# Optimization experiments

Measured on AMD Instinct MI355X. Metric: run time of the kernel, lower is better.

Reference implementation:

```python
import jax, jax.numpy as jnp
import numpy as np

N, C, H, W = 8, 80, 200, 200
PRE_NMS_THRESH = 0.05
PRE_NMS_TOP_N = 1000
NMS_THRESH = 0.6
FPN_POST_NMS_TOP_N = 100
MIN_SIZE = 0.0
TO_REMOVE = 1.0
CLASS_OFFSET = 100000.0  # > any coordinate; separates classes for class-aware NMS


def setup_inputs() -> dict:
    key = jax.random.key(0)
    k1, k2, k3, k4, k5 = jax.random.split(key, 5)
    # logits shifted so sigmoid probs sit near the 0.05 threshold (realistic sparsity)
    box_cls = jax.random.normal(k1, (N, C, H, W), jnp.float32) - 3.0
    box_regression = jax.random.uniform(k2, (N, 4, H, W), jnp.float32) * 64.0
    centerness = jax.random.normal(k3, (N, 1, H, W), jnp.float32)
    locations = jax.random.uniform(k4, (H * W, 2), jnp.float32) * 1600.0
    image_sizes = jax.random.randint(k5, (N, 2), 800, 1600, jnp.int32)  # (h, w)
    return {"locations": locations, "box_cls": box_cls,
            "box_regression": box_regression, "centerness": centerness,
            "image_sizes": image_sizes}


def _pairwise_iou(boxes):
    x1, y1, x2, y2 = boxes[:, 0], boxes[:, 1], boxes[:, 2], boxes[:, 3]
    area = (x2 - x1 + TO_REMOVE) * (y2 - y1 + TO_REMOVE)  # [K]
    iw = jnp.clip(jnp.minimum(x2[:, None], x2[None, :]) - jnp.maximum(x1[:, None], x1[None, :]) + TO_REMOVE, 0.0)
    ih = jnp.clip(jnp.minimum(y2[:, None], y2[None, :]) - jnp.maximum(y1[:, None], y1[None, :]) + TO_REMOVE, 0.0)
    inter = iw * ih
    return inter / (area[:, None] + area[None, :] - inter)


def reference(locations, box_cls, box_regression, centerness, image_sizes):
    n, c, h, w = box_cls.shape
    # [N,C,H,W] -> [N,HW,C] probs; [N,4,H,W] -> [N,HW,4]; centerness -> [N,HW]
    cls_prob = jax.nn.sigmoid(box_cls.transpose(0, 2, 3, 1).reshape(n, -1, c))
    reg = box_regression.transpose(0, 2, 3, 1).reshape(n, -1, 4)
    cent = jax.nn.sigmoid(centerness.transpose(0, 2, 3, 1).reshape(n, -1))

    def per_image(p, r, ct, hw):
        # candidate mask on raw class probs (before centerness weighting), as in source
        cand = p > PRE_NMS_THRESH                      # [HW, C]
        scores = p * ct[:, None]                       # [HW, C]
        flat = jnp.where(cand, scores, -jnp.inf).reshape(-1)
        top_s, top_i = jax.lax.top_k(flat, PRE_NMS_TOP_N)   # sorted desc
        loc_idx = top_i // c
        labels = top_i % c + 1
        valid = top_s > 0.0
        l2 = locations[loc_idx]                        # [K, 2]
        rr = r[loc_idx]                                # [K, 4]
        boxes = jnp.concatenate([l2 - rr[:, :2], l2 + rr[:, 2:]], axis=-1)
        ih = hw[0].astype(jnp.float32)
        iw = hw[1].astype(jnp.float32)
        boxes = jnp.stack([jnp.clip(boxes[:, 0], 0.0, iw - 1.0),
                           jnp.clip(boxes[:, 1], 0.0, ih - 1.0),
                           jnp.clip(boxes[:, 2], 0.0, iw - 1.0),
                           jnp.clip(boxes[:, 3], 0.0, ih - 1.0)], axis=-1)
        bw = boxes[:, 2] - boxes[:, 0] + TO_REMOVE
        bh = boxes[:, 3] - boxes[:, 1] + TO_REMOVE
        valid = valid & (bw >= MIN_SIZE) & (bh >= MIN_SIZE)
        # class-aware NMS via per-class coordinate offset
        ob = boxes + labels.astype(jnp.float32)[:, None] * CLASS_OFFSET
        iou = _pairwise_iou(ob)                        # [K, K]
        K = PRE_NMS_TOP_N
        idxs = jnp.arange(K)
        def body(supp, i):
            keep_i = valid[i] & jnp.logical_not(supp[i])
            supp = supp | (keep_i & (iou[i] > NMS_THRESH) & (idxs != i))
            return supp, keep_i
        _, keep = jax.lax.scan(body, jnp.zeros(K, dtype=bool), idxs)
        fscores = jnp.where(keep & valid, top_s, -jnp.inf)
        fs, fi = jax.lax.top_k(fscores, FPN_POST_NMS_TOP_N)
        fv = fs > 0.0
        fb = boxes[fi] * fv[:, None].astype(boxes.dtype)
        fl = jnp.where(fv, labels[fi], 0).astype(jnp.float32)
        out_s = jnp.where(fv, jnp.sqrt(jnp.where(fv, fs, 1.0)), 0.0)  # sqrt of cls*centerness
        # [K_post, 6] = x1,y1,x2,y2,score,label
        return jnp.concatenate([fb, out_s[:, None], fl[:, None]], axis=-1)

    return jax.vmap(per_image)(cls_prob, reg, cent, image_sizes)
```

## Files before the change

### kernel.cpp

```cpp
#include <hip/hip_runtime.h>
#include <math.h>

#define NIMG 8
#define NCLS 80
#define HW 40000
#define M (NCLS*HW)
#define UBINS 4096
#define CANDL 4096
#define SPILL_CAP 65536
#define BCAP 1024
#define TOPK 1000
#define OUTK 100
#define PRE_T 0.05f
#define NMS_T 0.6f
#define FLOOR_S 0.25f
#define FLOOR_BITS 0x3E800000u
#define FLOOR_SAFE 0.2494f

__device__ unsigned int       g_scnt[NIMG][32];
__device__ unsigned int       g_ovf[NIMG];
__device__ float              g_xthr[NIMG * HW];
__device__ float              g_sct[NIMG * HW];
__device__ unsigned long long g_key[NIMG][SPILL_CAP];

__device__ __forceinline__ float sigmoid_exact(float x){
    return 1.0f / (1.0f + expf(-x));
}

__device__ __forceinline__ unsigned long long shfl_xor_u64(unsigned long long v, int j){
    int lo = __shfl_xor((int)(unsigned int)(v & 0xffffffffull), j);
    int hi = __shfl_xor((int)(unsigned int)(v >> 32), j);
    return ((unsigned long long)(unsigned int)hi << 32) | (unsigned long long)(unsigned int)lo;
}

__global__ void k0_init(const float* __restrict__ cent){
    int t = blockIdx.x * blockDim.x + threadIdx.x;
    if (t < NIMG * 32) ((unsigned int*)g_scnt)[t] = 0u;
    if (t < NIMG) g_ovf[t] = 0u;
    if (t < NIMG * HW){
        float pct = sigmoid_exact(cent[t]);
        g_sct[t] = pct;
        float a = FLOOR_SAFE / pct;
        float xt;
        if (a >= 1.0f) xt = 3.0e38f;
        else {
            float am = fminf(a, 0.98f);
            xt = logf(am / (1.0f - am));
        }
        g_xthr[t] = xt;
    }
}

__global__ void __launch_bounds__(1024) k1_spill(const float* __restrict__ cls){
    const int n   = blockIdx.y;
    const int tid = threadIdx.x;
    const int e0  = blockIdx.x * 4096 + tid * 4;
    __shared__ unsigned long long skey[BCAP];
    __shared__ unsigned int lcnt, lbase;
    if (tid == 0) lcnt = 0u;
    __syncthreads();
    if (e0 < M){
        const int c  = e0 / HW;
        const int hw = e0 - c * HW;
        float4 x  = *(const float4*)(cls + (size_t)n * M + e0);
        float4 th = *(const float4*)(g_xthr + n * HW + hw);
        #define SPILL1(J, XV) \
        if (XV >= (J==0?th.x:J==1?th.y:J==2?th.z:th.w)){ \
            float p_ = sigmoid_exact(XV); \
            if (p_ > PRE_T){ \
                float s_ = p_ * g_sct[n * HW + hw + J]; \
                unsigned long long key_ = ((unsigned long long)__float_as_uint(s_) << 32) \
                    | (unsigned long long)(0xFFFFFFFFu - (unsigned int)((hw + J) * NCLS + c)); \
                unsigned int pp_ = atomicAdd(&lcnt, 1u); \
                if (pp_ < BCAP) skey[pp_] = key_; \
            } \
        }
        SPILL1(0, x.x)
        SPILL1(1, x.y)
        SPILL1(2, x.z)
        SPILL1(3, x.w)
        #undef SPILL1
    }
    __syncthreads();
    unsigned int raw = lcnt;
    unsigned int cnt = raw < BCAP ? raw : BCAP;
    if (tid == 0){
        lbase = cnt ? atomicAdd(&g_scnt[n][0], cnt) : 0u;
        if (raw > BCAP) g_ovf[n] = 1u;
    }
    __syncthreads();
    unsigned int base = lbase;
    for (unsigned int i = tid; i < cnt; i += 1024){
        unsigned int pos = base + i;
        if (pos < SPILL_CAP) g_key[n][pos] = skey[i];
    }
}

struct SelPhase {
    unsigned int hist[UBINS];
    unsigned int cs[256];
    unsigned long long keysL[CANDL];
};
struct NmsPhase {
    float ox1[TOPK], oy1[TOPK], ox2[TOPK], oy2[TOPK], oar[TOPK];
    float bxs[TOPK][4];
    float sc[TOPK];
    int   lab[TOPK];
    int   keeplist[OUTK];
    unsigned int  Wc[16][80];
    unsigned int  ctot[80];
    unsigned int  coff[81];
    unsigned int  wcnt[16];
    unsigned short ord[1024];
    unsigned char validf[TOPK];
    unsigned char supp[TOPK];
    unsigned char keepf[1024];
};
union KU { SelPhase sel; NmsPhase nms; };

#define REGSTEP(K_, J_) { \
    unsigned long long pa = shfl_xor_u64(va, (J_)); \
    unsigned long long pb = shfl_xor_u64(vb, (J_)); \
    bool fa = ((tid & (J_)) == 0); \
    bool da = ((tid & (K_)) == 0); \
    bool db = (((tid + 1024) & (K_)) == 0); \
    va = (fa == da) ? (va > pa ? va : pa) : (va < pa ? va : pa); \
    vb = (fa == db) ? (vb > pb ? vb : pb) : (vb < pb ? vb : pb); \
}

__global__ void __launch_bounds__(1024) k2_select_nms(const float* __restrict__ cls,
                                                      const float* __restrict__ loc,
                                                      const float* __restrict__ reg,
                                                      const int*   __restrict__ imsz,
                                                      float* __restrict__ out){
    const int n = blockIdx.x;
    const int tid = threadIdx.x;
    const int lane = tid & 63;
    const int wv   = tid >> 6;
    __shared__ KU u;
    __shared__ unsigned long long stop[TOPK];
    __shared__ unsigned int lcnt, c025, s_cut, s_flag, s_nmsfb, s_cnt, s_aok;

    if (tid == 0){ s_nmsfb = 0u; }

    unsigned int scnt_raw = g_scnt[n][0];
    unsigned int ovf_f    = g_ovf[n];
    unsigned int S = scnt_raw < SPILL_CAP ? scnt_raw : SPILL_CAP;

    bool modeA = (!ovf_f) && (scnt_raw >= TOPK) && (scnt_raw <= 2048);
    unsigned long long kk = 0ull;
    bool needBC = true;

    if (modeA){
        unsigned long long va = ((unsigned int)tid < S) ? g_key[n][tid] : 0ull;
        unsigned long long vb = ((unsigned int)(tid + 1024) < S) ? g_key[n][tid + 1024] : 0ull;

        REGSTEP(2,1)
        REGSTEP(4,2)  REGSTEP(4,1)
        REGSTEP(8,4)  REGSTEP(8,2)  REGSTEP(8,1)
        REGSTEP(16,8) REGSTEP(16,4) REGSTEP(16,2) REGSTEP(16,1)
        REGSTEP(32,16) REGSTEP(32,8) REGSTEP(32,4) REGSTEP(32,2) REGSTEP(32,1)
        REGSTEP(64,32) REGSTEP(64,16) REGSTEP(64,8) REGSTEP(64,4) REGSTEP(64,2) REGSTEP(64,1)

        for (int k = 128; k <= 2048; k <<= 1){
            if (k == 2048){
                unsigned long long mx = va > vb ? va : vb;
                unsigned long long mn = va > vb ? vb : va;
                va = mx; vb = mn;
            }
            u.sel.keysL[tid] = va; u.sel.keysL[tid + 1024] = vb;
            __syncthreads();
            for (int j = (k == 2048) ? 512 : (k >> 1); j >= 64; j >>= 1){
                int i  = ((tid & ~(j - 1)) << 1) | (tid & (j - 1));
                int l  = i | j;
                unsigned long long a = u.sel.keysL[i];
                unsigned long long b = u.sel.keysL[l];
                bool up = ((i & k) == 0);
                if (up ? (a < b) : (a > b)){ u.sel.keysL[i] = b; u.sel.keysL[l] = a; }
                __syncthreads();
            }
            va = u.sel.keysL[tid]; vb = u.sel.keysL[tid + 1024];
            REGSTEP(k,32) REGSTEP(k,16) REGSTEP(k,8) REGSTEP(k,4) REGSTEP(k,2) REGSTEP(k,1)
        }
        if (tid == TOPK - 1) s_aok = (((unsigned int)(va >> 32)) >= FLOOR_BITS) ? 1u : 0u;
        kk = (tid < TOPK) ? va : 0ull;
        __syncthreads();
        needBC = (s_aok == 0u);
    }

    if (needBC){
        for (int i = tid; i < UBINS; i += 1024) u.sel.hist[i] = 0u;
        if (tid == 0){ lcnt = 0u; c025 = 0u; }
        if (tid < TOPK) stop[tid] = 0ull;
        __syncthreads();

        for (unsigned int i = tid; i < S; i += 1024){
            unsigned long long k = g_key[n][i];
            unsigned int bits = (unsigned int)(k >> 32);
            float s = __uint_as_float(bits);
            int bin = (int)(s * 4096.0f);
            atomicAdd(&u.sel.hist[bin], 1u);
            unsigned long long mb = __ballot(bits >= FLOOR_BITS);
            if (lane == 0 && mb) atomicAdd(&c025, (unsigned int)__popcll(mb));
        }
        __syncthreads();
        if (tid < 256){
            unsigned int s = 0;
            int base = tid * 16;
            #pragma unroll
            for (int i = 0; i < 16; ++i) s += u.sel.hist[base + i];
            u.sel.cs[tid] = s;
        }
        __syncthreads();
        if (tid == 0){
            unsigned int acc = 0; int cut = 0;
            int c = 255;
            for (; c >= 0; --c){ if (acc + u.sel.cs[c] >= TOPK) break; acc += u.sel.cs[c]; }
            unsigned int Cest = 0;
            if (c >= 0){
                int b = c*16 + 15;
                for (;; --b){
                    if (acc + u.sel.hist[b] >= TOPK || b == c*16){ cut = b; break; }
                    acc += u.sel.hist[b];
                }
                Cest = acc + u.sel.hist[cut];
            }
            unsigned int fl = (scnt_raw > SPILL_CAP) || ovf_f || (c < 0) ||
                              (c025 < TOPK) || (Cest > CANDL) ? 1u : 0u;
            s_cut = (unsigned int)cut; s_flag = fl;
        }
        __syncthreads();

        if (s_flag){
            for (int i = tid; i < UBINS; i += 1024) u.sel.hist[i] = 0u;
            __syncthreads();
            const float* cls_n = cls + (size_t)n * M;
            const float* sct_n = g_sct + n * HW;
            for (int e = tid; e < M; e += 1024){
                float p = sigmoid_exact(cls_n[e]);
                if (p > PRE_T){
                    int c = e / HW; int hw = e - c * HW;
                    float s = p * sct_n[hw];
                    atomicAdd(&u.sel.hist[(int)(s * 4096.0f)], 1u);
                }
            }
            __syncthreads();
            if (tid < 256){
                unsigned int s = 0;
                int base = tid * 16;
                #pragma unroll
                for (int i = 0; i < 16; ++i) s += u.sel.hist[base + i];
                u.sel.cs[tid] = s;
            }
            __syncthreads();
            if (tid == 0){
                unsigned int acc = 0; int cut = 0; int c = 255;
                for (; c >= 0; --c){ if (acc + u.sel.cs[c] >= TOPK) break; acc += u.sel.cs[c]; }
                if (c >= 0){
                    int b = c*16 + 15;
                    for (;; --b){ acc += u.sel.hist[b]; if (acc >= TOPK || b == c*16) break; }
                    cut = b;
                }
                while (acc > CANDL && cut < UBINS){ acc -= u.sel.hist[cut]; cut++; }
                s_cut = (unsigned int)cut;
            }
            __syncthreads();
            unsigned int cutb = s_cut;
            for (int e = tid; e < M; e += 1024){
                float p = sigmoid_exact(cls_n[e]);
                if (p > PRE_T){
                    int c = e / HW; int hw = e - c * HW;
                    float s = p * sct_n[hw];
                    if ((int)(s * 4096.0f) >= (int)cutb){
                        unsigned int pos = atomicAdd(&lcnt, 1u);
                        if (pos < CANDL){
                            unsigned int idx = (unsigned int)(hw * NCLS + c);
                            u.sel.keysL[pos] = ((unsigned long long)__float_as_uint(s) << 32)
                                             | (unsigned long long)(0xFFFFFFFFu - idx);
                        }
                    }
                }
            }
        } else {
            unsigned int cutb = s_cut;
            for (unsigned int i = tid; i < S; i += 1024){
                unsigned long long k = g_key[n][i];
                float s = __uint_as_float((unsigned int)(k >> 32));
                bool pass = ((unsigned int)(int)(s * 4096.0f)) >= cutb;
                unsigned long long mb = __ballot(pass);
                unsigned int wcnt_ = (unsigned int)__popcll(mb);
                unsigned int base = 0;
                if (lane == 0 && wcnt_) base = atomicAdd(&lcnt, wcnt_);
                base = (unsigned int)__builtin_amdgcn_readfirstlane((int)base);
                if (pass){
                    unsigned int p = base + (unsigned int)__popcll(mb & ((1ull << lane) - 1ull));
                    if (p < CANDL) u.sel.keysL[p] = k;
                }
            }
        }
        __syncthreads();

        int C = (int)(lcnt < CANDL ? lcnt : CANDL);
        if (C <= 2048){
            int Nsort = (C <= 1024) ? 1024 : 2048;
            for (int i = C + tid; i < Nsort; i += 1024) u.sel.keysL[i] = 0ull;
            __syncthreads();
            for (int k = 2; k <= Nsort; k <<= 1){
                for (int j = k >> 1; j > 0; j >>= 1){
                    if (tid < (Nsort >> 1)){
                        int i  = ((tid & ~(j - 1)) << 1) | (tid & (j - 1));
                        int p2 = i | j;
                        unsigned long long a = u.sel.keysL[i];
                        unsigned long long b = u.sel.keysL[p2];
                        bool up = ((i & k) == 0);
                        if (up ? (a < b) : (a > b)){ u.sel.keysL[i] = b; u.sel.keysL[p2] = a; }
                    }
                    __syncthreads();
                }
            }
            if (tid < TOPK) stop[tid] = u.sel.keysL[tid];
        } else {
            for (int i = tid; i < C; i += 1024){
                unsigned long long k = u.sel.keysL[i];
                int rank = 0;
                for (int j = 0; j < C; ++j) rank += (u.sel.keysL[j] > k) ? 1 : 0;
                if (rank < TOPK) stop[rank] = k;
            }
        }
        __syncthreads();
        kk = (tid < TOPK) ? stop[tid] : 0ull;
        __syncthreads();
    }

    float rx1 = 0.f, ry1 = 0.f, rx2 = -1.f, ry2 = -1.f, rar = 1.f;
    float ihh = (float)imsz[2*n + 0];
    float iww = (float)imsz[2*n + 1];

    u.nms.keepf[tid] = 0;
    { unsigned int* wz = &u.nms.Wc[0][0];
      for (int i = tid; i < 16*80; i += 1024) wz[i] = 0u; }

    if (tid < TOPK){
        unsigned int bits = (unsigned int)(kk >> 32);
        float s = __uint_as_float(bits);
        u.nms.supp[tid] = 0;
        if (s > 0.0f){
            unsigned int idx = 0xFFFFFFFFu - (unsigned int)(kk & 0xFFFFFFFFull);
            int hw = (int)(idx / NCLS);
            int c  = (int)(idx % NCLS);
            int l  = c + 1;
            float x  = loc[2*hw], y = loc[2*hw + 1];
            float r0 = reg[((size_t)n*4 + 0)*HW + hw];
            float r1 = reg[((size_t)n*4 + 1)*HW + hw];
            float r2 = reg[((size_t)n*4 + 2)*HW + hw];
            float r3 = reg[((size_t)n*4 + 3)*HW + hw];
            float x1 = fminf(fmaxf(x - r0, 0.0f), iww - 1.0f);
            float y1 = fminf(fmaxf(y - r1, 0.0f), ihh - 1.0f);
            float x2 = fminf(fmaxf(x + r2, 0.0f), iww - 1.0f);
            float y2 = fminf(fmaxf(y + r3, 0.0f), ihh - 1.0f);
            u.nms.bxs[tid][0] = x1; u.nms.bxs[tid][1] = y1;
            u.nms.bxs[tid][2] = x2; u.nms.bxs[tid][3] = y2;
            float off = (float)l * 100000.0f;
            float a1 = x1 + off, b1 = y1 + off, a2 = x2 + off, b2 = y2 + off;
            float ar = (a2 - a1 + 1.0f) * (b2 - b1 + 1.0f);
            u.nms.ox1[tid] = a1; u.nms.oy1[tid] = b1;
            u.nms.ox2[tid] = a2; u.nms.oy2[tid] = b2; u.nms.oar[tid] = ar;
            rx1 = a1; ry1 = b1; rx2 = a2; ry2 = b2; rar = ar;
            u.nms.sc[tid] = s; u.nms.lab[tid] = l; u.nms.validf[tid] = 1;
        } else {
            u.nms.validf[tid] = 0; u.nms.sc[tid] = 0.0f; u.nms.lab[tid] = 0;
            u.nms.bxs[tid][0] = u.nms.bxs[tid][1] = 0.0f;
            u.nms.bxs[tid][2] = u.nms.bxs[tid][3] = 0.0f;
            u.nms.ox1[tid] = 0.f; u.nms.oy1[tid] = 0.f;
            u.nms.ox2[tid] = -1.f; u.nms.oy2[tid] = -1.f; u.nms.oar[tid] = 1.f;
        }
    }
    __syncthreads();

    int mk = -1;
    if (tid < TOPK && u.nms.validf[tid]) mk = u.nms.lab[tid] - 1;
    if (mk >= 0) atomicAdd(&u.nms.Wc[wv][mk], 1u);
    __syncthreads();
    if (tid < NCLS){
        unsigned int acc = 0;
        for (int w = 0; w < 16; ++w){
            unsigned int v = u.nms.Wc[w][tid];
            u.nms.Wc[w][tid] = acc;
            acc += v;
        }
        u.nms.ctot[tid] = acc;
        if (acc > 64) atomicOr(&s_nmsfb, 1u);
    }
    __syncthreads();
    if (tid <= NCLS){
        unsigned int acc = 0;
        for (int kq = 0; kq < tid; ++kq) acc += u.nms.ctot[kq];
        u.nms.coff[tid] = acc;
    }
    __syncthreads();

    if (!s_nmsfb){
        int below = 0;
        for (int l = 0; l < 64; ++l){
            int ok = __shfl(mk, l);
            below += (l < lane && ok == mk) ? 1 : 0;
        }
        if (mk >= 0){
            unsigned int pos = u.nms.coff[mk] + u.nms.Wc[wv][mk] + (unsigned int)below;
            u.nms.ord[pos] = (unsigned short)tid;
        }
        __syncthreads();

        for (int k = wv; k < NCLS; k += 16){
            int base = (int)u.nms.coff[k];
            int ck   = (int)u.nms.coff[k + 1] - base;
            if (ck <= 0) continue;
            int rr = (lane < ck) ? (int)u.nms.ord[base + lane] : -1;
            float bx1 = 0.f, by1 = 0.f, bx2 = -1.f, by2 = -1.f, bar = 1.f;
            if (rr >= 0){
                bx1 = u.nms.ox1[rr]; by1 = u.nms.oy1[rr];
                bx2 = u.nms.ox2[rr]; by2 = u.nms.oy2[rr]; bar = u.nms.oar[rr];
            }
            int sup = 0;
            for (int p = 0; p < ck; ++p){
                int keep_p = !__shfl(sup, p);
                if (keep_p){
                    float px1 = __shfl(bx1, p), py1 = __shfl(by1, p);
                    float px2 = __shfl(bx2, p), py2 = __shfl(by2, p);
                    float par = __shfl(bar, p);
                    if (lane > p && rr >= 0){
                        float ix1 = fmaxf(px1, bx1);
                        float iy1 = fmaxf(py1, by1);
                        float ix2 = fminf(px2, bx2);
                        float iy2 = fminf(py2, by2);
                        float iw_ = fmaxf(ix2 - ix1 + 1.0f, 0.0f);
                        float ih_ = fmaxf(iy2 - iy1 + 1.0f, 0.0f);
                        float inter = iw_ * ih_;
                        float iou = inter / (par + bar - inter);
                        if (iou > NMS_T) sup = 1;
                    }
                }
            }
            if (rr >= 0) u.nms.keepf[rr] = sup ? 0 : 1;
        }
        __syncthreads();

        int kf = (int)u.nms.keepf[tid];
        unsigned long long mb = __ballot(kf != 0);
        if (lane == 0) u.nms.wcnt[wv] = (unsigned int)__popcll(mb);
        __syncthreads();
        if (wv == 0){
            unsigned int v = (lane < 16) ? u.nms.wcnt[lane] : 0u;
            unsigned int orig = v;
            for (int d = 1; d < 16; d <<= 1){
                unsigned int t = __shfl_up(v, d);
                if (lane >= d) v += t;
            }
            if (lane < 16) u.nms.wcnt[lane] = v - orig;
            if (lane == 15) s_cnt = (v < OUTK ? v : OUTK);
        }
        __syncthreads();
        if (kf){
            unsigned int slot = u.nms.wcnt[wv] + (unsigned int)__popcll(mb & ((1ull << lane) - 1ull));
            if (slot < OUTK) u.nms.keeplist[slot] = tid;
        }
    } else {
        int cnt = 0;
        for (int i = 0; i < TOPK; ++i){
            bool keep_i = u.nms.validf[i] && !u.nms.supp[i];
            if (keep_i){
                if (tid == 0) u.nms.keeplist[cnt] = i;
                if (tid < TOPK && tid != i){
                    float ix1 = fmaxf(u.nms.ox1[i], rx1);
                    float iy1 = fmaxf(u.nms.oy1[i], ry1);
                    float ix2 = fminf(u.nms.ox2[i], rx2);
                    float iy2 = fminf(u.nms.oy2[i], ry2);
                    float iw_ = fmaxf(ix2 - ix1 + 1.0f, 0.0f);
                    float ih_ = fmaxf(iy2 - iy1 + 1.0f, 0.0f);
                    float inter = iw_ * ih_;
                    float iou = inter / (u.nms.oar[i] + rar - inter);
                    if (iou > NMS_T) u.nms.supp[tid] = 1;
                }
                cnt++;
                __syncthreads();
                if (cnt == OUTK) break;
            }
        }
        if (tid == 0) s_cnt = (unsigned int)(cnt < OUTK ? cnt : OUTK);
    }
    __syncthreads();

    int cnt = (int)s_cnt;
    if (tid < OUTK){
        float r0=0.f,r1=0.f,r2=0.f,r3=0.f,r4=0.f,r5=0.f;
        if (tid < cnt){
            int i = u.nms.keeplist[tid];
            r0 = u.nms.bxs[i][0]; r1 = u.nms.bxs[i][1];
            r2 = u.nms.bxs[i][2]; r3 = u.nms.bxs[i][3];
            r4 = sqrtf(u.nms.sc[i]); r5 = (float)u.nms.lab[i];
        }
        float* o = out + ((size_t)n*OUTK + tid)*6;
        o[0]=r0; o[1]=r1; o[2]=r2; o[3]=r3; o[4]=r4; o[5]=r5;
    }
}

extern "C" void kernel_launch(void* const* d_in, const int* in_sizes, int n_in,
                              void* d_out, int out_size, void* d_ws, size_t ws_size,
                              hipStream_t stream){
    const float* loc  = (const float*)d_in[0];
    const float* cls  = (const float*)d_in[1];
    const float* reg  = (const float*)d_in[2];
    const float* cent = (const float*)d_in[3];
    const int*   imsz = (const int*)d_in[4];
    float* out = (float*)d_out;

    hipLaunchKernelGGL(k0_init,       dim3(625),                 dim3(512),  0, stream, cent);
    hipLaunchKernelGGL(k1_spill,      dim3((M+4095)/4096, NIMG), dim3(1024), 0, stream, cls);
    hipLaunchKernelGGL(k2_select_nms, dim3(NIMG),                dim3(1024), 0, stream,
                       cls, loc, reg, imsz, out);
}
```

Measured before the change: 254.6 us.

## Unify selection path with parallel histogram scans and sort-verify fallback

Restructures top-K selection so the spilled-key histogram and cutoff search always run first. Serial single-thread scans for the bin cutoff and class offsets become wave-level shuffle prefix sums. Candidates above the cutoff are then sorted with the register/LDS hybrid bitonic sort, followed by a sortedness check that falls back to the full shared-memory bitonic sort if needed. This drops the speculative mode-A path and its floor re-check, trading an extra histogram pass for fewer serial loops and fewer divergent code paths.

```diff
diff --git a/kernel.cpp b/kernel.cpp
--- a/kernel.cpp
+++ b/kernel.cpp
@@ -13,7 +13,6 @@
 #define OUTK 100
 #define PRE_T 0.05f
 #define NMS_T 0.6f
-#define FLOOR_S 0.25f
 #define FLOOR_BITS 0x3E800000u
 #define FLOOR_SAFE 0.2494f
 
@@ -99,6 +98,7 @@
 struct SelPhase {
     unsigned int hist[UBINS];
     unsigned int cs[256];
+    unsigned int wtot[4];
     unsigned long long keysL[CANDL];
 };
 struct NmsPhase {
@@ -139,29 +139,158 @@
     const int wv   = tid >> 6;
     __shared__ KU u;
     __shared__ unsigned long long stop[TOPK];
-    __shared__ unsigned int lcnt, c025, s_cut, s_flag, s_nmsfb, s_cnt, s_aok;
-
-    if (tid == 0){ s_nmsfb = 0u; }
+    __shared__ unsigned int lcnt, s_cut, s_flag, s_nmsfb, s_cnt, s_c, s_csn, s_Cest, s_srtbad;
+
+    for (int i = tid; i < UBINS; i += 1024) u.sel.hist[i] = 0u;
+    if (tid == 0){ s_nmsfb = 0u; s_srtbad = 0u; s_c = 0xFFFFFFFFu; s_csn = 0u;
+                   s_Cest = 0u; s_cut = 0u; lcnt = 0u; }
+    if (tid < TOPK) stop[tid] = 0ull;
+    __syncthreads();
 
     unsigned int scnt_raw = g_scnt[n][0];
     unsigned int ovf_f    = g_ovf[n];
     unsigned int S = scnt_raw < SPILL_CAP ? scnt_raw : SPILL_CAP;
 
-    bool modeA = (!ovf_f) && (scnt_raw >= TOPK) && (scnt_raw <= 2048);
+    for (unsigned int i = tid; i < S; i += 1024){
+        unsigned long long k = g_key[n][i];
+        float s = __uint_as_float((unsigned int)(k >> 32));
+        atomicAdd(&u.sel.hist[(int)(s * 4096.0f)], 1u);
+    }
+    __syncthreads();
+    if (tid < 256){
+        unsigned int s = 0;
+        int base = tid * 16;
+        #pragma unroll
+        for (int i = 0; i < 16; ++i) s += u.sel.hist[base + i];
+        u.sel.cs[tid] = s;
+    }
+    __syncthreads();
+    if (tid < 256){
+        unsigned int v = u.sel.cs[tid];
+        #pragma unroll
+        for (int d = 1; d < 64; d <<= 1){
+            unsigned int t = __shfl_down(v, d);
+            if (lane + d < 64) v += t;
+        }
+        if (lane == 0) u.sel.wtot[wv] = v;
+        u.sel.cs[tid] = v;
+    }
+    __syncthreads();
+    if (tid < 256){
+        unsigned int tail = 0;
+        for (int w = wv + 1; w < 4; ++w) tail += u.sel.wtot[w];
+        u.sel.cs[tid] += tail;
+    }
+    __syncthreads();
+    if (tid < 256){
+        unsigned int a = u.sel.cs[tid];
+        unsigned int b = (tid == 255) ? 0u : u.sel.cs[tid + 1];
+        if (a >= TOPK && b < TOPK){ s_c = (unsigned int)tid; s_csn = b; }
+    }
+    __syncthreads();
+    if (wv == 0 && s_c != 0xFFFFFFFFu){
+        unsigned int cst = s_c;
+        unsigned int h = (lane < 16) ? u.sel.hist[cst * 16 + lane] : 0u;
+        #pragma unroll
+        for (int d = 1; d < 16; d <<= 1){
+            unsigned int t = __shfl_down(h, d);
+            if (lane + d < 16) h += t;
+        }
+        unsigned int gs  = h + s_csn;
+        unsigned int gsn = __shfl_down(gs, 1);
+        if (lane == 15) gsn = s_csn;
+        if (lane < 16 && gs >= TOPK && gsn < TOPK){ s_cut = cst * 16 + lane; s_Cest = gs; }
+    }
+    __syncthreads();
+    if (tid == 0){
+        unsigned int c025 = u.sel.cs[64];
+        s_flag = (scnt_raw > SPILL_CAP) || ovf_f || (s_c == 0xFFFFFFFFu) ||
+                 (c025 < TOPK) || (s_Cest > CANDL) ? 1u : 0u;
+    }
+    __syncthreads();
+
+    if (s_flag){
+        for (int i = tid; i < UBINS; i += 1024) u.sel.hist[i] = 0u;
+        __syncthreads();
+        const float* cls_n = cls + (size_t)n * M;
+        const float* sct_n = g_sct + n * HW;
+        for (int e = tid; e < M; e += 1024){
+            float p = sigmoid_exact(cls_n[e]);
+            if (p > PRE_T){
+                int c = e / HW; int hw = e - c * HW;
+                float s = p * sct_n[hw];
+                atomicAdd(&u.sel.hist[(int)(s * 4096.0f)], 1u);
+            }
+        }
+        __syncthreads();
+        if (tid < 256){
+            unsigned int s = 0;
+            int base = tid * 16;
+            #pragma unroll
+            for (int i = 0; i < 16; ++i) s += u.sel.hist[base + i];
+            u.sel.cs[tid] = s;
+        }
+        __syncthreads();
+        if (tid == 0){
+            unsigned int acc = 0; int cut = 0; int c = 255;
+            for (; c >= 0; --c){ if (acc + u.sel.cs[c] >= TOPK) break; acc += u.sel.cs[c]; }
+            if (c >= 0){
+                int b = c*16 + 15;
+                for (;; --b){ acc += u.sel.hist[b]; if (acc >= TOPK || b == c*16) break; }
+                cut = b;
+            }
+            while (acc > CANDL && cut < UBINS){ acc -= u.sel.hist[cut]; cut++; }
+            s_cut = (unsigned int)cut;
+        }
+        __syncthreads();
+        unsigned int cutb = s_cut;
+        for (int e = tid; e < M; e += 1024){
+            float p = sigmoid_exact(cls_n[e]);
+            if (p > PRE_T){
+                int c = e / HW; int hw = e - c * HW;
+                float s = p * sct_n[hw];
+                if ((int)(s * 4096.0f) >= (int)cutb){
+                    unsigned int pos = atomicAdd(&lcnt, 1u);
+                    if (pos < CANDL){
+                        unsigned int idx = (unsigned int)(hw * NCLS + c);
+                        u.sel.keysL[pos] = ((unsigned long long)__float_as_uint(s) << 32)
+                                         | (unsigned long long)(0xFFFFFFFFu - idx);
+                    }
+                }
+            }
+        }
+    } else {
+        unsigned int cutb = s_cut;
+        for (unsigned int i = tid; i < S; i += 1024){
+            unsigned long long k = g_key[n][i];
+            float s = __uint_as_float((unsigned int)(k >> 32));
+            bool pass = ((unsigned int)(int)(s * 4096.0f)) >= cutb;
+            unsigned long long mb = __ballot(pass);
+            unsigned int wcnt_ = (unsigned int)__popcll(mb);
+            unsigned int base = 0;
+            if (lane == 0 && wcnt_) base = atomicAdd(&lcnt, wcnt_);
+            base = (unsigned int)__builtin_amdgcn_readfirstlane((int)base);
+            if (pass){
+                unsigned int p = base + (unsigned int)__popcll(mb & ((1ull << lane) - 1ull));
+                if (p < CANDL) u.sel.keysL[p] = k;
+            }
+        }
+    }
+    __syncthreads();
+
+    int C = (int)(lcnt < CANDL ? lcnt : CANDL);
     unsigned long long kk = 0ull;
-    bool needBC = true;
-
-    if (modeA){
-        unsigned long long va = ((unsigned int)tid < S) ? g_key[n][tid] : 0ull;
-        unsigned long long vb = ((unsigned int)(tid + 1024) < S) ? g_key[n][tid + 1024] : 0ull;
-
+    if (C <= 2048){
+        for (int i = C + tid; i < 2048; i += 1024) u.sel.keysL[i] = 0ull;
+        __syncthreads();
+        unsigned long long va = u.sel.keysL[tid];
+        unsigned long long vb = u.sel.keysL[tid + 1024];
         REGSTEP(2,1)
         REGSTEP(4,2)  REGSTEP(4,1)
         REGSTEP(8,4)  REGSTEP(8,2)  REGSTEP(8,1)
         REGSTEP(16,8) REGSTEP(16,4) REGSTEP(16,2) REGSTEP(16,1)
         REGSTEP(32,16) REGSTEP(32,8) REGSTEP(32,4) REGSTEP(32,2) REGSTEP(32,1)
         REGSTEP(64,32) REGSTEP(64,16) REGSTEP(64,8) REGSTEP(64,4) REGSTEP(64,2) REGSTEP(64,1)
-
         for (int k = 128; k <= 2048; k <<= 1){
             if (k == 2048){
                 unsigned long long mx = va > vb ? va : vb;
@@ -172,165 +301,88 @@
             __syncthreads();
             for (int j = (k == 2048) ? 512 : (k >> 1); j >= 64; j >>= 1){
                 int i  = ((tid & ~(j - 1)) << 1) | (tid & (j - 1));
-                int l  = i | j;
+                int p2 = i | j;
                 unsigned long long a = u.sel.keysL[i];
-                unsigned long long b = u.sel.keysL[l];
+                unsigned long long b = u.sel.keysL[p2];
                 bool up = ((i & k) == 0);
-                if (up ? (a < b) : (a > b)){ u.sel.keysL[i] = b; u.sel.keysL[l] = a; }
+                if (up ? (a < b) : (a > b)){ u.sel.keysL[i] = b; u.sel.keysL[p2] = a; }
                 __syncthreads();
             }
             va = u.sel.keysL[tid]; vb = u.sel.keysL[tid + 1024];
             REGSTEP(k,32) REGSTEP(k,16) REGSTEP(k,8) REGSTEP(k,4) REGSTEP(k,2) REGSTEP(k,1)
         }
-        if (tid == TOPK - 1) s_aok = (((unsigned int)(va >> 32)) >= FLOOR_BITS) ? 1u : 0u;
-        kk = (tid < TOPK) ? va : 0ull;
-        __syncthreads();
-        needBC = (s_aok == 0u);
-    }
-
-    if (needBC){
-        for (int i = tid; i < UBINS; i += 1024) u.sel.hist[i] = 0u;
-        if (tid == 0){ lcnt = 0u; c025 = 0u; }
-        if (tid < TOPK) stop[tid] = 0ull;
-        __syncthreads();
-
-        for (unsigned int i = tid; i < S; i += 1024){
-            unsigned long long k = g_key[n][i];
-            unsigned int bits = (unsigned int)(k >> 32);
-            float s = __uint_as_float(bits);
-            int bin = (int)(s * 4096.0f);
-            atomicAdd(&u.sel.hist[bin], 1u);
-            unsigned long long mb = __ballot(bits >= FLOOR_BITS);
-            if (lane == 0 && mb) atomicAdd(&c025, (unsigned int)__popcll(mb));
-        }
-        __syncthreads();
-        if (tid < 256){
-            unsigned int s = 0;
-            int base = tid * 16;
-            #pragma unroll
-            for (int i = 0; i < 16; ++i) s += u.sel.hist[base + i];
-            u.sel.cs[tid] = s;
-        }
-        __syncthreads();
-        if (tid == 0){
-            unsigned int acc = 0; int cut = 0;
-            int c = 255;
-            for (; c >= 0; --c){ if (acc + u.sel.cs[c] >= TOPK) break; acc += u.sel.cs[c]; }
-            unsigned int Cest = 0;
-            if (c >= 0){
-                int b = c*16 + 15;
-                for (;; --b){
-                    if (acc + u.sel.hist[b] >= TOPK || b == c*16){ cut = b; break; }
-                    acc += u.sel.hist[b];
-                }
-                Cest = acc + u.sel.hist[cut];
-            }
-            unsigned int fl = (scnt_raw > SPILL_CAP) || ovf_f || (c < 0) ||
-                              (c025 < TOPK) || (Cest > CANDL) ? 1u : 0u;
-            s_cut = (unsigned int)cut; s_flag = fl;
-        }
-        __syncthreads();
-
-        if (s_flag){
-            for (int i = tid; i < UBINS; i += 1024) u.sel.hist[i] = 0u;
-            __syncthreads();
-            const float* cls_n = cls + (size_t)n * M;
-            const float* sct_n = g_sct + n * HW;
-            for (int e = tid; e < M; e += 1024){
-                float p = sigmoid_exact(cls_n[e]);
-                if (p > PRE_T){
-                    int c = e / HW; int hw = e - c * HW;
-                    float s = p * sct_n[hw];
-                    atomicAdd(&u.sel.hist[(int)(s * 4096.0f)], 1u);
-                }
-            }
-            __syncthreads();
-            if (tid < 256){
-                unsigned int s = 0;
-                int base = tid * 16;
-                #pragma unroll
-                for (int i = 0; i < 16; ++i) s += u.sel.hist[base + i];
-                u.sel.cs[tid] = s;
-            }
-            __syncthreads();
-            if (tid == 0){
-                unsigned int acc = 0; int cut = 0; int c = 255;
-                for (; c >= 0; --c){ if (acc + u.sel.cs[c] >= TOPK) break; acc += u.sel.cs[c]; }
-                if (c >= 0){
-                    int b = c*16 + 15;
-                    for (;; --b){ acc += u.sel.hist[b]; if (acc >= TOPK || b == c*16) break; }
-                    cut = b;
-                }
-                while (acc > CANDL && cut < UBINS){ acc -= u.sel.hist[cut]; cut++; }
-                s_cut = (unsigned int)cut;
-            }
+        u.sel.keysL[tid] = va; u.sel.keysL[tid + 1024] = vb;
+        __syncthreads();
+        bool bad = (u.sel.keysL[tid] < u.sel.keysL[tid + 1]);
+        if (tid <= 1022) bad = bad || (u.sel.keysL[tid + 1024] < u.sel.keysL[tid + 1025]);
+        if (bad) atomicOr(&s_srtbad, 1u);
+        __syncthreads();
+        if (s_srtbad){
+            if (tid == 0) lcnt = 0u;
             __syncthreads();
             unsigned int cutb = s_cut;
-            for (int e = tid; e < M; e += 1024){
-                float p = sigmoid_exact(cls_n[e]);
-                if (p > PRE_T){
-                    int c = e / HW; int hw = e - c * HW;
-                    float s = p * sct_n[hw];
-                    if ((int)(s * 4096.0f) >= (int)cutb){
-                        unsigned int pos = atomicAdd(&lcnt, 1u);
-                        if (pos < CANDL){
-                            unsigned int idx = (unsigned int)(hw * NCLS + c);
-                            u.sel.keysL[pos] = ((unsigned long long)__float_as_uint(s) << 32)
-                                             | (unsigned long long)(0xFFFFFFFFu - idx);
+            if (s_flag){
+                const float* cls_n = cls + (size_t)n * M;
+                const float* sct_n = g_sct + n * HW;
+                for (int e = tid; e < M; e += 1024){
+                    float p = sigmoid_exact(cls_n[e]);
+                    if (p > PRE_T){
+                        int c = e / HW; int hw = e - c * HW;
+                        float s = p * sct_n[hw];
+                        if ((int)(s * 4096.0f) >= (int)cutb){
+                            unsigned int pos = atomicAdd(&lcnt, 1u);
+                            if (pos < CANDL){
+                                unsigned int idx = (unsigned int)(hw * NCLS + c);
+                                u.sel.keysL[pos] = ((unsigned long long)__float_as_uint(s) << 32)
+                                                 | (unsigned long long)(0xFFFFFFFFu - idx);
+                            }
                         }
                     }
                 }
-            }
-        } else {
-            unsigned int cutb = s_cut;
-            for (unsigned int i = tid; i < S; i += 1024){
-                unsigned long long k = g_key[n][i];
-                float s = __uint_as_float((unsigned int)(k >> 32));
-                bool pass = ((unsigned int)(int)(s * 4096.0f)) >= cutb;
-                unsigned long long mb = __ballot(pass);
-                unsigned int wcnt_ = (unsigned int)__popcll(mb);
-                unsigned int base = 0;
-                if (lane == 0 && wcnt_) base = atomicAdd(&lcnt, wcnt_);
-                base = (unsigned int)__builtin_amdgcn_readfirstlane((int)base);
-                if (pass){
-                    unsigned int p = base + (unsigned int)__popcll(mb & ((1ull << lane) - 1ull));
-                    if (p < CANDL) u.sel.keysL[p] = k;
+            } else {
+                for (unsigned int i = tid; i < S; i += 1024){
+                    unsigned long long k = g_key[n][i];
+                    float s = __uint_as_float((unsigned int)(k >> 32));
+                    bool pass = ((unsigned int)(int)(s * 4096.0f)) >= cutb;
+                    unsigned long long mb = __ballot(pass);
+                    unsigned int wcnt_ = (unsigned int)__popcll(mb);
+                    unsigned int base = 0;
+                    if (lane == 0 && wcnt_) base = atomicAdd(&lcnt, wcnt_);
+                    base = (unsigned int)__builtin_amdgcn_readfirstlane((int)base);
+                    if (pass){
+                        unsigned int p = base + (unsigned int)__popcll(mb & ((1ull << lane) - 1ull));
+                        if (p < CANDL) u.sel.keysL[p] = k;
+                    }
                 }
             }
-        }
-        __syncthreads();
-
-        int C = (int)(lcnt < CANDL ? lcnt : CANDL);
-        if (C <= 2048){
-            int Nsort = (C <= 1024) ? 1024 : 2048;
-            for (int i = C + tid; i < Nsort; i += 1024) u.sel.keysL[i] = 0ull;
             __syncthreads();
-            for (int k = 2; k <= Nsort; k <<= 1){
+            int C2 = (int)(lcnt < CANDL ? lcnt : CANDL);
+            for (int i = C2 + tid; i < 2048; i += 1024) u.sel.keysL[i] = 0ull;
+            __syncthreads();
+            for (int k = 2; k <= 2048; k <<= 1){
                 for (int j = k >> 1; j > 0; j >>= 1){
-                    if (tid < (Nsort >> 1)){
-                        int i  = ((tid & ~(j - 1)) << 1) | (tid & (j - 1));
-                        int p2 = i | j;
-                        unsigned long long a = u.sel.keysL[i];
-                        unsigned long long b = u.sel.keysL[p2];
-                        bool up = ((i & k) == 0);
-                        if (up ? (a < b) : (a > b)){ u.sel.keysL[i] = b; u.sel.keysL[p2] = a; }
-                    }
+                    int i  = ((tid & ~(j - 1)) << 1) | (tid & (j - 1));
+                    int p2 = i | j;
+                    unsigned long long a = u.sel.keysL[i];
+                    unsigned long long b = u.sel.keysL[p2];
+                    bool up = ((i & k) == 0);
+                    if (up ? (a < b) : (a > b)){ u.sel.keysL[i] = b; u.sel.keysL[p2] = a; }
                     __syncthreads();
                 }
             }
-            if (tid < TOPK) stop[tid] = u.sel.keysL[tid];
-        } else {
-            for (int i = tid; i < C; i += 1024){
-                unsigned long long k = u.sel.keysL[i];
-                int rank = 0;
-                for (int j = 0; j < C; ++j) rank += (u.sel.keysL[j] > k) ? 1 : 0;
-                if (rank < TOPK) stop[rank] = k;
-            }
+        }
+        kk = (tid < TOPK) ? u.sel.keysL[tid] : 0ull;
+    } else {
+        for (int i = tid; i < C; i += 1024){
+            unsigned long long k = u.sel.keysL[i];
+            int rank = 0;
+            for (int j = 0; j < C; ++j) rank += (u.sel.keysL[j] > k) ? 1 : 0;
+            if (rank < TOPK) stop[rank] = k;
         }
         __syncthreads();
         kk = (tid < TOPK) ? stop[tid] : 0ull;
-        __syncthreads();
-    }
+    }
+    __syncthreads();
 
     float rx1 = 0.f, ry1 = 0.f, rx2 = -1.f, ry2 = -1.f, rar = 1.f;
     float ihh = (float)imsz[2*n + 0];
@@ -392,10 +444,24 @@
         if (acc > 64) atomicOr(&s_nmsfb, 1u);
     }
     __syncthreads();
-    if (tid <= NCLS){
-        unsigned int acc = 0;
-        for (int kq = 0; kq < tid; ++kq) acc += u.nms.ctot[kq];
-        u.nms.coff[tid] = acc;
+    if (wv == 0){
+        unsigned int v = u.nms.ctot[lane];
+        unsigned int inc = v;
+        #pragma unroll
+        for (int d = 1; d < 64; d <<= 1){
+            unsigned int t = __shfl_up(inc, d);
+            if (lane >= d) inc += t;
+        }
+        u.nms.coff[lane + 1] = inc;
+        if (lane == 0) u.nms.coff[0] = 0u;
+        unsigned int base = __shfl(inc, 63);
+        unsigned int inc2 = (lane < 16) ? u.nms.ctot[64 + lane] : 0u;
+        #pragma unroll
+        for (int d = 1; d < 16; d <<= 1){
+            unsigned int t = __shfl_up(inc2, d);
+            if (lane >= d) inc2 += t;
+        }
+        if (lane < 16) u.nms.coff[65 + lane] = base + inc2;
     }
     __syncthreads();
 
```

Result: no change. 257.0 us (+0.9%).
